# Performance work log

Hardware: AMD Instinct MI355X
Metric: run time of the kernel (lower is better)

Reference implementation:

```python
import jax, jax.numpy as jnp
import numpy as np

DT = 0.01
T, B, I, H, O = 512, 128, 256, 1024, 256


def setup_inputs() -> dict:
    key = jax.random.key(0)
    ks = jax.random.split(key, 9)
    def xavier(k, out_f, in_f):
        lim = np.sqrt(6.0 / (in_f + out_f)).astype(np.float32)
        return jax.random.uniform(k, (out_f, in_f), jnp.float32, -lim, lim)
    return {
        "x": jax.random.normal(ks[0], (T, B, I), jnp.float32),
        "W_h": xavier(ks[1], H, I + H),                      # HRCell linear, no bias
        "gain": jnp.ones((H,), jnp.float32),
        "omega": jax.random.uniform(ks[2], (H,), jnp.float32, 10.0, 50.0),
        "b_offset": jax.random.uniform(ks[3], (H,), jnp.float32, 1.0, 6.0),
        "W_o": xavier(ks[4], H, H),                          # LICell linear, no bias
        "tau_mem": 20.0 + 5.0 * jax.random.normal(ks[5], (H,), jnp.float32),
        "W_out": xavier(ks[6], O, H),                        # readout Linear
        "b_out": jnp.zeros((O,), jnp.float32),
    }


def reference(x, W_h, gain, omega, b_offset, W_o, tau_mem, W_out, b_out):
    om = jnp.abs(omega)
    om2 = om * om
    b = om2 * 0.005 + jnp.abs(b_offset)          # damping coefficient per unit
    alpha = jnp.exp(-1.0 / jnp.abs(tau_mem))     # leaky-integrator decay
    Bsz = x.shape[1]
    Hd = W_h.shape[0]
    Od = W_out.shape[0]

    def step(carry, x_t):
        hu, hv, ou, acc = carry
        # HRCell: linear on concat(input, hidden_u), then harmonic update
        in_sum = jnp.concatenate([x_t, hu], axis=1) @ W_h.T   # [B, H]
        hv = hv + hu * DT
        hu = hu + in_sum * DT - b * hu * (2.0 * DT) - om2 * hv * DT
        hu = hu * gain                                        # normalize=False path
        # LICell: leaky integrator on projected hidden
        ou = ou * alpha + (hu @ W_o.T) * (1.0 - alpha)
        # readout, summed over time
        acc = acc + ou @ W_out.T + b_out
        return (hu, hv, ou, acc), None

    z = jnp.zeros((Bsz, Hd), x.dtype)
    init = (z, z, z, jnp.zeros((Bsz, Od), x.dtype))
    (hu, hv, ou, acc), _ = jax.lax.scan(step, init, x)
    return acc
```

## Files before the change

kernel.cpp:

```cpp
#include <hip/hip_runtime.h>
#include <math.h>

#define DT 0.01f
constexpr int T = 512, B = 128, I = 256, H = 1024, O = 256;
constexpr int K = I + H;

constexpr size_t OFF_OSUM  = 0;
constexpr size_t OFF_HUH0  = OFF_OSUM + (size_t)B * H;
constexpr size_t OFF_HUL0  = OFF_HUH0 + (size_t)B * H / 2;
constexpr size_t OFF_HUH1  = OFF_HUL0 + (size_t)B * H / 2;
constexpr size_t OFF_HUL1  = OFF_HUH1 + (size_t)B * H / 2;
constexpr size_t OFF_COEF  = OFF_HUL1 + (size_t)B * H / 2;
constexpr size_t OFF_FLAGS = OFF_COEF + 5 * (size_t)H;
constexpr size_t OFF_WHH   = OFF_FLAGS + 8256;
constexpr size_t OFF_WHL   = OFF_WHH + 64 * 40 * 64 * 8 / 2;
constexpr size_t OFF_WOH   = OFF_WHL + 64 * 40 * 64 * 8 / 2;
constexpr size_t OFF_WOL   = OFF_WOH + 64 * 32 * 64 * 8 / 2;

constexpr int SM_WHH  = 0;
constexpr int SM_WHL  = 65536;
constexpr int SM_REDS = 131072;
constexpr int SM_REDP = 139520;
constexpr int SM_BYTES = 147968;

typedef __attribute__((ext_vector_type(8))) short short8v;
typedef __attribute__((ext_vector_type(4))) float f32x4;

static __device__ inline short f2bf(float f) {
    unsigned u = __builtin_bit_cast(unsigned, f);
    u += 0x7fffu + ((u >> 16) & 1u);
    return (short)(u >> 16);
}
static __device__ inline float bf2f(short s) {
    return __builtin_bit_cast(float, ((unsigned)(unsigned short)s) << 16);
}

__global__ __launch_bounds__(256)
void init_kernel(float* __restrict__ ws, const float* __restrict__ omega,
                 const float* __restrict__ b_offset, const float* __restrict__ tau_mem,
                 const float* __restrict__ gain) {
    size_t tid = (size_t)blockIdx.x * blockDim.x + threadIdx.x;
    size_t stride = (size_t)gridDim.x * blockDim.x;
    for (size_t i = tid; i < (size_t)B * H; i += stride) ws[OFF_HUH0 + i] = 0.0f;
    for (size_t i = tid; i < 8256; i += stride) ws[OFF_FLAGS + i] = 0.0f;
    if (tid < H) {
        float om  = fabsf(omega[tid]);
        float om2 = om * om;
        float bb  = om2 * 0.005f + fabsf(b_offset[tid]);
        float al  = expf(-1.0f / fabsf(tau_mem[tid]));
        float g   = gain[tid];
        ws[OFF_COEF + 0 * H + tid] = g * (1.0f - 2.0f * bb * DT);
        ws[OFF_COEF + 1 * H + tid] = g * DT;
        ws[OFF_COEF + 2 * H + tid] = g * om2 * DT;
        ws[OFF_COEF + 3 * H + tid] = al;
        ws[OFF_COEF + 4 * H + tid] = 1.0f - al;
    }
}

template <int NKS, int KD>
__global__ __launch_bounds__(256)
void convert_kernel(const float* __restrict__ W, short* __restrict__ WH,
                    short* __restrict__ WL) {
    int g = blockIdx.x * 256 + threadIdx.x;
    int lane = g & 63;
    int ks = (g >> 6) % NKS;
    int cg = g / (NKS * 64);
    int col = cg * 16 + (lane & 15);
    int k = ks * 32 + ((lane >> 4) << 3);
    const float* src = W + (size_t)col * KD + k;
    short8v hi, lo;
    #pragma unroll
    for (int j = 0; j < 8; ++j) {
        float v = src[j];
        short h = f2bf(v);
        hi[j] = h;
        lo[j] = f2bf(v - bf2f(h));
    }
    *(short8v*)(WH + (size_t)g * 8) = hi;
    *(short8v*)(WL + (size_t)g * 8) = lo;
}

__global__ __launch_bounds__(512)
void rnn_persist(const float* __restrict__ x, float* __restrict__ ws) {
    extern __shared__ char sm[];
    float* redS = (float*)(sm + SM_REDS);
    float* redP = (float*)(sm + SM_REDP);
    __shared__ int role_sm;

    const float* coef = ws + OFF_COEF;
    float* osum_g = ws + OFF_OSUM;
    const short* huhS[2] = {(const short*)(ws + OFF_HUH0), (const short*)(ws + OFF_HUH1)};
    const short* hulS[2] = {(const short*)(ws + OFF_HUL0), (const short*)(ws + OFF_HUL1)};
    unsigned int* huhW[2] = {(unsigned int*)(ws + OFF_HUH0), (unsigned int*)(ws + OFF_HUH1)};
    unsigned int* hulW[2] = {(unsigned int*)(ws + OFF_HUL0), (unsigned int*)(ws + OFF_HUL1)};
    int* flags = (int*)(ws + OFF_FLAGS);
    int* ctr   = flags + 8192;

    const int tid = threadIdx.x;

    if (tid == 0) {
        unsigned xcc_;
        asm volatile("s_getreg_b32 %0, hwreg(HW_REG_XCC_ID)" : "=s"(xcc_));
        int slot = atomicAdd(ctr + (xcc_ & 7), 1);
        role_sm = (int)((xcc_ & 7) * 32 + (slot & 31));
    }
    __syncthreads();
    const int role = role_sm;
    const int xcc = role >> 5;
    const int g   = role & 31;
    const int col0 = g * 32, row0 = xcc * 16;

    const int wid = tid >> 6, lane = tid & 63;
    const int ntile = wid & 1, ksl = wid >> 1;
    const int colgrp = 2 * g + ntile;
    const int rowg = row0 + (lane & 15);
    const int koff = (lane >> 4) << 3;

    {
        const float4* srcH = (const float4*)(ws + OFF_WHH);
        const float4* srcL = (const float4*)(ws + OFF_WHL);
        float4* dH = (float4*)(sm + SM_WHH);
        float4* dL = (float4*)(sm + SM_WHL);
        for (int i = tid; i < 2 * 2048; i += 512) {
            int n = i >> 11, rem = i & 2047;
            dH[i] = srcH[((size_t)(2 * g + n) * 40 + 8) * 64 + rem];
            dL[i] = srcL[((size_t)(2 * g + n) * 40 + 8) * 64 + rem];
        }
    }
    short8v woh[8], wxh[2], wxl[2];
    {
        const short8v* WOHg = (const short8v*)(ws + OFF_WOH) + (size_t)colgrp * 32 * 64 + lane;
        const short8v* WXH  = (const short8v*)(ws + OFF_WHH) + (size_t)colgrp * 40 * 64 + lane;
        const short8v* WXL  = (const short8v*)(ws + OFF_WHL) + (size_t)colgrp * 40 * 64 + lane;
        #pragma unroll
        for (int j = 0; j < 8; ++j) woh[j] = WOHg[(ksl * 8 + j) * 64];
        #pragma unroll
        for (int j = 0; j < 2; ++j) { wxh[j] = WXH[(ksl * 2 + j) * 64]; wxl[j] = WXL[(ksl * 2 + j) * 64]; }
    }
    __syncthreads();

    const short8v* lWHH = (const short8v*)(sm + SM_WHH) + (size_t)ntile * 2048 + lane;
    const short8v* lWHL = (const short8v*)(sm + SM_WHL) + (size_t)ntile * 2048 + lane;

    const int er = tid >> 4;
    const int ec0 = (tid & 15) * 2;
    const int gcol0 = col0 + ec0;
    const size_t erow = (size_t)(row0 + (er & 15));
    float k1a=0,k1b=0,k2a=0,k2b=0,k3a=0,k3b=0, ala=0,alb=0,alma=0,almb=0;
    if (tid < 256) {
        k1a = coef[gcol0];         k1b = coef[gcol0 + 1];
        k2a = coef[H + gcol0];     k2b = coef[H + gcol0 + 1];
        k3a = coef[2 * H + gcol0]; k3b = coef[2 * H + gcol0 + 1];
        ala = coef[3 * H + gcol0]; alb = coef[3 * H + gcol0 + 1];
        alma = coef[4 * H + gcol0]; almb = coef[4 * H + gcol0 + 1];
    }
    float hva=0,hvb=0,oua=0,oub=0,osa=0,osb=0,hua=0,hub=0;

    int* myfast = flags + ((xcc * 32 + g) << 4);
    int* mysafe = flags + 4096 + ((xcc * 32 + g) << 4);
    const int* fastp = flags + ((xcc * 32 + (tid & 31)) << 4);
    int* safep = flags + 4096 + ((xcc * 32 + (tid & 31)) << 4);
    const size_t rowOffH = (size_t)rowg * H + koff;

    for (int s = 0; s <= T; ++s) {
        const bool last = (s == T);
        f32x4 accS = {0,0,0,0}, accS2 = {0,0,0,0};
        f32x4 accP = {0,0,0,0}, accP2 = {0,0,0,0};

        if (!last) {
            const float* xrow = x + (size_t)s * B * I + (size_t)rowg * I + koff;
            #pragma unroll
            for (int j = 0; j < 2; ++j) {
                float4 a0 = *(const float4*)(xrow + (ksl * 2 + j) * 32);
                float4 a1 = *(const float4*)(xrow + (ksl * 2 + j) * 32 + 4);
                float av[8] = {a0.x,a0.y,a0.z,a0.w,a1.x,a1.y,a1.z,a1.w};
                short8v ah, alv;
                #pragma unroll
                for (int q = 0; q < 8; ++q) {
                    short h = f2bf(av[q]);
                    ah[q] = h;
                    alv[q] = f2bf(av[q] - bf2f(h));
                }
                f32x4* acc = j ? &accS2 : &accS;
                *acc = __builtin_amdgcn_mfma_f32_16x16x32_bf16(ah, wxh[j], *acc, 0,0,0);
                *acc = __builtin_amdgcn_mfma_f32_16x16x32_bf16(alv, wxh[j], *acc, 0,0,0);
                *acc = __builtin_amdgcn_mfma_f32_16x16x32_bf16(ah, wxl[j], *acc, 0,0,0);
            }
        }

        if (tid < 32) {
            int v, spins = 0;
            for (;;) {
                asm volatile("global_load_dword %0, %1, off sc0\n\ts_waitcnt vmcnt(0)"
                             : "=v"(v) : "v"(fastp) : "memory");
                if (v >= s) break;
                if ((++spins & 63) == 0) {
                    v = __hip_atomic_load(safep, __ATOMIC_RELAXED, __HIP_MEMORY_SCOPE_AGENT);
                    if (v >= s) break;
                }
                __builtin_amdgcn_s_sleep(1);
            }
        }
        __syncthreads();
        asm volatile("" ::: "memory");

        const short* hb_ = huhS[s & 1] + rowOffH;
        const short* lb_ = hulS[s & 1] + rowOffH;
        short8v hbuf[8], lbuf[8];
        #pragma unroll
        for (int j = 0; j < 8; ++j) {
            asm volatile("global_load_dwordx4 %0, %1, off sc0" : "=v"(hbuf[j]) : "v"(hb_ + (ksl * 8 + j) * 32));
            asm volatile("global_load_dwordx4 %0, %1, off sc0" : "=v"(lbuf[j]) : "v"(lb_ + (ksl * 8 + j) * 32));
        }
        if (s > 0 && tid < 256) {
            const float* rp = redP + er * 33 + ec0;
            float p0 = (rp[0] + rp[528]) + (rp[1056] + rp[1584]);
            float p1 = (rp[1] + rp[529]) + (rp[1057] + rp[1585]);
            oua = oua * ala + p0 * alma; osa += oua;
            oub = oub * alb + p1 * almb; osb += oub;
        }

        if (!last) {
            asm volatile("s_waitcnt vmcnt(8)");
            __builtin_amdgcn_sched_barrier(0);
            #pragma unroll
            for (int j = 0; j < 4; ++j) {
                short8v ch = lWHH[(ksl * 8 + j) * 64];
                short8v cl = lWHL[(ksl * 8 + j) * 64];
                f32x4* acc = (j & 1) ? &accS2 : &accS;
                *acc = __builtin_amdgcn_mfma_f32_16x16x32_bf16(hbuf[j], ch, *acc, 0,0,0);
                *acc = __builtin_amdgcn_mfma_f32_16x16x32_bf16(lbuf[j], ch, *acc, 0,0,0);
                *acc = __builtin_amdgcn_mfma_f32_16x16x32_bf16(hbuf[j], cl, *acc, 0,0,0);
            }
            asm volatile("s_waitcnt vmcnt(0)");
            __builtin_amdgcn_sched_barrier(0);
            #pragma unroll
            for (int j = 4; j < 8; ++j) {
                short8v ch = lWHH[(ksl * 8 + j) * 64];
                short8v cl = lWHL[(ksl * 8 + j) * 64];
                f32x4* acc = (j & 1) ? &accS2 : &accS;
                *acc = __builtin_amdgcn_mfma_f32_16x16x32_bf16(hbuf[j], ch, *acc, 0,0,0);
                *acc = __builtin_amdgcn_mfma_f32_16x16x32_bf16(lbuf[j], ch, *acc, 0,0,0);
                *acc = __builtin_amdgcn_mfma_f32_16x16x32_bf16(hbuf[j], cl, *acc, 0,0,0);
            }
            #pragma unroll
            for (int r = 0; r < 4; ++r) {
                int crow = ((lane >> 4) << 2) + r;
                redS[ksl * 528 + crow * 33 + ntile * 16 + (lane & 15)] = accS[r] + accS2[r];
            }
            __syncthreads();

            if (tid < 256) {
                const float* rs = redS + er * 33 + ec0;
                float s0 = (rs[0] + rs[528]) + (rs[1056] + rs[1584]);
                float s1 = (rs[1] + rs[529]) + (rs[1057] + rs[1585]);
                float hvn0 = hva + hua * DT;
                float hun0 = k1a * hua + k2a * s0 - k3a * hvn0;
                hva = hvn0; hua = hun0;
                float hvn1 = hvb + hub * DT;
                float hun1 = k1b * hub + k2b * s1 - k3b * hvn1;
                hvb = hvn1; hub = hun1;
                short h0 = f2bf(hun0), h1 = f2bf(hun1);
                short l0 = f2bf(hun0 - bf2f(h0)), l1 = f2bf(hun1 - bf2f(h1));
                unsigned hp = (unsigned)(unsigned short)h0 | ((unsigned)(unsigned short)h1 << 16);
                unsigned lp = (unsigned)(unsigned short)l0 | ((unsigned)(unsigned short)l1 << 16);
                size_t off32 = (erow * H + gcol0) >> 1;
                unsigned int* hp_ = huhW[(s + 1) & 1] + off32;
                unsigned int* lp_ = hulW[(s + 1) & 1] + off32;
                asm volatile("global_store_dword %0, %1, off sc0" :: "v"(hp_), "v"(hp) : "memory");
                asm volatile("global_store_dword %0, %1, off sc0" :: "v"(lp_), "v"(lp) : "memory");
            }
            asm volatile("s_waitcnt vmcnt(0)" ::: "memory");
            __syncthreads();
            if (tid == 0) {
                int fv = s + 1;
                asm volatile("global_store_dword %0, %1, off sc0" :: "v"(myfast), "v"(fv) : "memory");
                __hip_atomic_store(mysafe, fv, __ATOMIC_RELAXED, __HIP_MEMORY_SCOPE_AGENT);
            }
        } else {
            asm volatile("s_waitcnt vmcnt(0)");
            __builtin_amdgcn_sched_barrier(0);
            __syncthreads();
        }

        #pragma unroll
        for (int j = 0; j < 8; ++j) {
            f32x4* acc = (j & 1) ? &accP2 : &accP;
            *acc = __builtin_amdgcn_mfma_f32_16x16x32_bf16(hbuf[j], woh[j], *acc, 0,0,0);
            *acc = __builtin_amdgcn_mfma_f32_16x16x32_bf16(lbuf[j], woh[j], *acc, 0,0,0);
        }
        #pragma unroll
        for (int r = 0; r < 4; ++r) {
            int crow = ((lane >> 4) << 2) + r;
            redP[ksl * 528 + crow * 33 + ntile * 16 + (lane & 15)] = accP[r] + accP2[r];
        }
    }

    __syncthreads();
    if (tid < 256) {
        const float* rp = redP + er * 33 + ec0;
        float p0 = (rp[0] + rp[528]) + (rp[1056] + rp[1584]);
        float p1 = (rp[1] + rp[529]) + (rp[1057] + rp[1585]);
        float o0 = oua * ala + p0 * alma; osa += o0;
        float o1 = oub * alb + p1 * almb; osb += o1;
        osum_g[erow * H + gcol0] = osa;
        osum_g[erow * H + gcol0 + 1] = osb;
    }
}

__global__ __launch_bounds__(256)
void readout_kernel(const float* __restrict__ ou_sum, const float* __restrict__ W_out,
                    const float* __restrict__ b_out, float* __restrict__ out) {
    constexpr int KC = 128, BT = 32, CT = 16;
    __shared__ float act[BT][KC + 4];
    __shared__ float w[CT][KC + 4];
    int wg = blockIdx.x;
    int bt = wg & 3, cg = wg >> 2;
    int row0 = bt * BT, col0 = cg * CT;
    int tid = threadIdx.x;
    int c = tid & 15, rr = tid >> 4;

    float4 acc0 = {0, 0, 0, 0}, acc1 = {0, 0, 0, 0};
    for (int kc = 0; kc < H / KC; ++kc) {
        int k0 = kc * KC;
        for (int i = tid; i < BT * (KC / 4); i += 256) {
            int r = i >> 5, c4 = (i & 31) * 4;
            *(float4*)&act[r][c4] = *(const float4*)&ou_sum[(size_t)(row0 + r) * H + k0 + c4];
        }
        for (int i = tid; i < CT * (KC / 4); i += 256) {
            int r = i >> 5, c4 = (i & 31) * 4;
            *(float4*)&w[r][c4] = *(const float4*)&W_out[(size_t)(col0 + r) * H + k0 + c4];
        }
        __syncthreads();
        #pragma unroll
        for (int k4 = 0; k4 < KC / 4; ++k4) {
            float4 a0 = *(const float4*)&act[rr][k4 * 4];
            float4 a1 = *(const float4*)&act[rr + 16][k4 * 4];
            float4 w0 = *(const float4*)&w[c][k4 * 4];
            acc0.x = fmaf(a0.x, w0.x, acc0.x); acc0.y = fmaf(a0.y, w0.y, acc0.y);
            acc0.z = fmaf(a0.z, w0.z, acc0.z); acc0.w = fmaf(a0.w, w0.w, acc0.w);
            acc1.x = fmaf(a1.x, w0.x, acc1.x); acc1.y = fmaf(a1.y, w0.y, acc1.y);
            acc1.z = fmaf(a1.z, w0.z, acc1.z); acc1.w = fmaf(a1.w, w0.w, acc1.w);
        }
        __syncthreads();
    }
    float v0 = (acc0.x + acc0.y) + (acc0.z + acc0.w);
    float v1 = (acc1.x + acc1.y) + (acc1.z + acc1.w);
    int gcol = col0 + c;
    float bo = b_out[gcol] * (float)T;
    out[(size_t)(row0 + rr) * O + gcol] = v0 + bo;
    out[(size_t)(row0 + rr + 16) * O + gcol] = v1 + bo;
}

extern "C" void kernel_launch(void* const* d_in, const int* in_sizes, int n_in,
                              void* d_out, int out_size, void* d_ws, size_t ws_size,
                              hipStream_t stream) {
    const float* x        = (const float*)d_in[0];
    const float* W_h      = (const float*)d_in[1];
    const float* gain     = (const float*)d_in[2];
    const float* omega    = (const float*)d_in[3];
    const float* b_offset = (const float*)d_in[4];
    const float* W_o      = (const float*)d_in[5];
    const float* tau_mem  = (const float*)d_in[6];
    const float* W_out    = (const float*)d_in[7];
    const float* b_out    = (const float*)d_in[8];
    float* ws  = (float*)d_ws;
    float* out = (float*)d_out;

    init_kernel<<<512, 256, 0, stream>>>(ws, omega, b_offset, tau_mem, gain);
    convert_kernel<40, K><<<640, 256, 0, stream>>>(
        W_h, (short*)(ws + OFF_WHH), (short*)(ws + OFF_WHL));
    convert_kernel<32, H><<<512, 256, 0, stream>>>(
        W_o, (short*)(ws + OFF_WOH), (short*)(ws + OFF_WOL));

    rnn_persist<<<256, 512, SM_BYTES, stream>>>(x, ws);

    readout_kernel<<<64, 256, 0, stream>>>(ws + OFF_OSUM, W_out, b_out, out);
}
```

Before: 3.790 ms.

## Shrink persistent RNN blocks to two waves with full-K per wave and triple buffering

```diff
diff --git a/kernel.cpp b/kernel.cpp
--- a/kernel.cpp
+++ b/kernel.cpp
@@ -10,18 +10,16 @@
 constexpr size_t OFF_HUL0  = OFF_HUH0 + (size_t)B * H / 2;
 constexpr size_t OFF_HUH1  = OFF_HUL0 + (size_t)B * H / 2;
 constexpr size_t OFF_HUL1  = OFF_HUH1 + (size_t)B * H / 2;
-constexpr size_t OFF_COEF  = OFF_HUL1 + (size_t)B * H / 2;
+constexpr size_t OFF_HUH2  = OFF_HUL1 + (size_t)B * H / 2;
+constexpr size_t OFF_HUL2  = OFF_HUH2 + (size_t)B * H / 2;
+constexpr size_t OFF_COEF  = OFF_HUL2 + (size_t)B * H / 2;
 constexpr size_t OFF_FLAGS = OFF_COEF + 5 * (size_t)H;
-constexpr size_t OFF_WHH   = OFF_FLAGS + 8256;
+constexpr size_t OFF_WHH   = OFF_FLAGS + 9344;
 constexpr size_t OFF_WHL   = OFF_WHH + 64 * 40 * 64 * 8 / 2;
 constexpr size_t OFF_WOH   = OFF_WHL + 64 * 40 * 64 * 8 / 2;
 constexpr size_t OFF_WOL   = OFF_WOH + 64 * 32 * 64 * 8 / 2;
 
-constexpr int SM_WHH  = 0;
-constexpr int SM_WHL  = 65536;
-constexpr int SM_REDS = 131072;
-constexpr int SM_REDP = 139520;
-constexpr int SM_BYTES = 147968;
+constexpr int SM_BYTES = 131072;
 
 typedef __attribute__((ext_vector_type(8))) short short8v;
 typedef __attribute__((ext_vector_type(4))) float f32x4;
@@ -42,7 +40,7 @@
     size_t tid = (size_t)blockIdx.x * blockDim.x + threadIdx.x;
     size_t stride = (size_t)gridDim.x * blockDim.x;
     for (size_t i = tid; i < (size_t)B * H; i += stride) ws[OFF_HUH0 + i] = 0.0f;
-    for (size_t i = tid; i < 8256; i += stride) ws[OFF_FLAGS + i] = 0.0f;
+    for (size_t i = tid; i < 9344; i += stride) ws[OFF_FLAGS + i] = 0.0f;
     if (tid < H) {
         float om  = fabsf(omega[tid]);
         float om2 = om * om;
@@ -80,21 +78,21 @@
     *(short8v*)(WL + (size_t)g * 8) = lo;
 }
 
-__global__ __launch_bounds__(512)
+__global__ __launch_bounds__(128)
 void rnn_persist(const float* __restrict__ x, float* __restrict__ ws) {
     extern __shared__ char sm[];
-    float* redS = (float*)(sm + SM_REDS);
-    float* redP = (float*)(sm + SM_REDP);
     __shared__ int role_sm;
 
     const float* coef = ws + OFF_COEF;
     float* osum_g = ws + OFF_OSUM;
-    const short* huhS[2] = {(const short*)(ws + OFF_HUH0), (const short*)(ws + OFF_HUH1)};
-    const short* hulS[2] = {(const short*)(ws + OFF_HUL0), (const short*)(ws + OFF_HUL1)};
-    unsigned int* huhW[2] = {(unsigned int*)(ws + OFF_HUH0), (unsigned int*)(ws + OFF_HUH1)};
-    unsigned int* hulW[2] = {(unsigned int*)(ws + OFF_HUL0), (unsigned int*)(ws + OFF_HUL1)};
+    const short* huhS[3] = {(const short*)(ws + OFF_HUH0), (const short*)(ws + OFF_HUH1),
+                            (const short*)(ws + OFF_HUH2)};
+    const short* hulS[3] = {(const short*)(ws + OFF_HUL0), (const short*)(ws + OFF_HUL1),
+                            (const short*)(ws + OFF_HUL2)};
+    short* huhW[3] = {(short*)(ws + OFF_HUH0), (short*)(ws + OFF_HUH1), (short*)(ws + OFF_HUH2)};
+    short* hulW[3] = {(short*)(ws + OFF_HUL0), (short*)(ws + OFF_HUL1), (short*)(ws + OFF_HUL2)};
     int* flags = (int*)(ws + OFF_FLAGS);
-    int* ctr   = flags + 8192;
+    int* ctr   = flags + 9216;
 
     const int tid = threadIdx.x;
 
@@ -108,72 +106,60 @@
     const int role = role_sm;
     const int xcc = role >> 5;
     const int g   = role & 31;
-    const int col0 = g * 32, row0 = xcc * 16;
-
-    const int wid = tid >> 6, lane = tid & 63;
-    const int ntile = wid & 1, ksl = wid >> 1;
-    const int colgrp = 2 * g + ntile;
+    const int w   = tid >> 6, lane = tid & 63;
+    const int cg  = g * 2 + w;
+    const int col0 = cg * 16;
+    const int row0 = xcc * 16;
     const int rowg = row0 + (lane & 15);
     const int koff = (lane >> 4) << 3;
 
     {
         const float4* srcH = (const float4*)(ws + OFF_WHH);
         const float4* srcL = (const float4*)(ws + OFF_WHL);
-        float4* dH = (float4*)(sm + SM_WHH);
-        float4* dL = (float4*)(sm + SM_WHL);
-        for (int i = tid; i < 2 * 2048; i += 512) {
+        float4* dH = (float4*)sm;
+        float4* dL = (float4*)(sm + 65536);
+        for (int i = tid; i < 2 * 2048; i += 128) {
             int n = i >> 11, rem = i & 2047;
             dH[i] = srcH[((size_t)(2 * g + n) * 40 + 8) * 64 + rem];
             dL[i] = srcL[((size_t)(2 * g + n) * 40 + 8) * 64 + rem];
         }
     }
-    short8v woh[8], wxh[2], wxl[2];
+    short8v wxh[8], wxl[8];
     {
-        const short8v* WOHg = (const short8v*)(ws + OFF_WOH) + (size_t)colgrp * 32 * 64 + lane;
-        const short8v* WXH  = (const short8v*)(ws + OFF_WHH) + (size_t)colgrp * 40 * 64 + lane;
-        const short8v* WXL  = (const short8v*)(ws + OFF_WHL) + (size_t)colgrp * 40 * 64 + lane;
+        const short8v* WXH = (const short8v*)(ws + OFF_WHH) + (size_t)cg * 40 * 64 + lane;
+        const short8v* WXL = (const short8v*)(ws + OFF_WHL) + (size_t)cg * 40 * 64 + lane;
         #pragma unroll
-        for (int j = 0; j < 8; ++j) woh[j] = WOHg[(ksl * 8 + j) * 64];
-        #pragma unroll
-        for (int j = 0; j < 2; ++j) { wxh[j] = WXH[(ksl * 2 + j) * 64]; wxl[j] = WXL[(ksl * 2 + j) * 64]; }
+        for (int j = 0; j < 8; ++j) { wxh[j] = WXH[j * 64]; wxl[j] = WXL[j * 64]; }
     }
     __syncthreads();
 
-    const short8v* lWHH = (const short8v*)(sm + SM_WHH) + (size_t)ntile * 2048 + lane;
-    const short8v* lWHL = (const short8v*)(sm + SM_WHL) + (size_t)ntile * 2048 + lane;
-
-    const int er = tid >> 4;
-    const int ec0 = (tid & 15) * 2;
-    const int gcol0 = col0 + ec0;
-    const size_t erow = (size_t)(row0 + (er & 15));
-    float k1a=0,k1b=0,k2a=0,k2b=0,k3a=0,k3b=0, ala=0,alb=0,alma=0,almb=0;
-    if (tid < 256) {
-        k1a = coef[gcol0];         k1b = coef[gcol0 + 1];
-        k2a = coef[H + gcol0];     k2b = coef[H + gcol0 + 1];
-        k3a = coef[2 * H + gcol0]; k3b = coef[2 * H + gcol0 + 1];
-        ala = coef[3 * H + gcol0]; alb = coef[3 * H + gcol0 + 1];
-        alma = coef[4 * H + gcol0]; almb = coef[4 * H + gcol0 + 1];
-    }
-    float hva=0,hvb=0,oua=0,oub=0,osa=0,osb=0,hua=0,hub=0;
-
-    int* myfast = flags + ((xcc * 32 + g) << 4);
-    int* mysafe = flags + 4096 + ((xcc * 32 + g) << 4);
-    const int* fastp = flags + ((xcc * 32 + (tid & 31)) << 4);
-    int* safep = flags + 4096 + ((xcc * 32 + (tid & 31)) << 4);
-    const size_t rowOffH = (size_t)rowg * H + koff;
+    const short8v* lWHH = (const short8v*)sm + (size_t)w * 2048 + lane;
+    const short8v* lWHL = (const short8v*)(sm + 65536) + (size_t)w * 2048 + lane;
+    const short8v* WOH  = (const short8v*)(ws + OFF_WOH) + (size_t)cg * 32 * 64 + lane;
+
+    const int mycol = col0 + (lane & 15);
+    const int myrow0 = row0 + ((lane >> 4) << 2);
+    const float k1 = coef[mycol], k2 = coef[H + mycol], k3 = coef[2 * H + mycol];
+    const float al = coef[3 * H + mycol], alm = coef[4 * H + mycol];
+    float hu4[4] = {0,0,0,0}, hv4[4] = {0,0,0,0}, ou4[4] = {0,0,0,0}, os4[4] = {0,0,0,0};
+
+    int* myfast = flags + (xcc * 64 + cg);
+    int* mysafe = flags + 1024 + ((xcc * 64 + cg) << 4);
+    const int* pollfast = flags + (xcc * 64 + lane);
+    int* pollsafe = flags + 1024 + ((xcc * 64 + lane) << 4);
+    const size_t rowOff = (size_t)rowg * H + koff;
 
     for (int s = 0; s <= T; ++s) {
         const bool last = (s == T);
-        f32x4 accS = {0,0,0,0}, accS2 = {0,0,0,0};
-        f32x4 accP = {0,0,0,0}, accP2 = {0,0,0,0};
+        f32x4 a1 = {0,0,0,0}, a2 = {0,0,0,0}, a3 = {0,0,0,0};
 
         if (!last) {
             const float* xrow = x + (size_t)s * B * I + (size_t)rowg * I + koff;
             #pragma unroll
-            for (int j = 0; j < 2; ++j) {
-                float4 a0 = *(const float4*)(xrow + (ksl * 2 + j) * 32);
-                float4 a1 = *(const float4*)(xrow + (ksl * 2 + j) * 32 + 4);
-                float av[8] = {a0.x,a0.y,a0.z,a0.w,a1.x,a1.y,a1.z,a1.w};
+            for (int j = 0; j < 8; ++j) {
+                float4 q0 = *(const float4*)(xrow + j * 32);
+                float4 q1 = *(const float4*)(xrow + j * 32 + 4);
+                float av[8] = {q0.x,q0.y,q0.z,q0.w,q1.x,q1.y,q1.z,q1.w};
                 short8v ah, alv;
                 #pragma unroll
                 for (int q = 0; q < 8; ++q) {
@@ -181,131 +167,145 @@
                     ah[q] = h;
                     alv[q] = f2bf(av[q] - bf2f(h));
                 }
-                f32x4* acc = j ? &accS2 : &accS;
-                *acc = __builtin_amdgcn_mfma_f32_16x16x32_bf16(ah, wxh[j], *acc, 0,0,0);
-                *acc = __builtin_amdgcn_mfma_f32_16x16x32_bf16(alv, wxh[j], *acc, 0,0,0);
-                *acc = __builtin_amdgcn_mfma_f32_16x16x32_bf16(ah, wxl[j], *acc, 0,0,0);
-            }
-        }
-
-        if (tid < 32) {
+                a1 = __builtin_amdgcn_mfma_f32_16x16x32_bf16(ah,  wxh[j], a1, 0,0,0);
+                a2 = __builtin_amdgcn_mfma_f32_16x16x32_bf16(alv, wxh[j], a2, 0,0,0);
+                a3 = __builtin_amdgcn_mfma_f32_16x16x32_bf16(ah,  wxl[j], a3, 0,0,0);
+            }
+        }
+
+        {
             int v, spins = 0;
             for (;;) {
                 asm volatile("global_load_dword %0, %1, off sc0\n\ts_waitcnt vmcnt(0)"
-                             : "=v"(v) : "v"(fastp) : "memory");
-                if (v >= s) break;
+                             : "=v"(v) : "v"(pollfast) : "memory");
+                if (__all(v >= s)) break;
                 if ((++spins & 63) == 0) {
-                    v = __hip_atomic_load(safep, __ATOMIC_RELAXED, __HIP_MEMORY_SCOPE_AGENT);
-                    if (v >= s) break;
+                    int v2 = __hip_atomic_load(pollsafe, __ATOMIC_RELAXED, __HIP_MEMORY_SCOPE_AGENT);
+                    if (v2 > v) v = v2;
+                    if (__all(v >= s)) break;
                 }
                 __builtin_amdgcn_s_sleep(1);
             }
         }
-        __syncthreads();
         asm volatile("" ::: "memory");
 
-        const short* hb_ = huhS[s & 1] + rowOffH;
-        const short* lb_ = hulS[s & 1] + rowOffH;
-        short8v hbuf[8], lbuf[8];
-        #pragma unroll
-        for (int j = 0; j < 8; ++j) {
-            asm volatile("global_load_dwordx4 %0, %1, off sc0" : "=v"(hbuf[j]) : "v"(hb_ + (ksl * 8 + j) * 32));
-            asm volatile("global_load_dwordx4 %0, %1, off sc0" : "=v"(lbuf[j]) : "v"(lb_ + (ksl * 8 + j) * 32));
-        }
-        if (s > 0 && tid < 256) {
-            const float* rp = redP + er * 33 + ec0;
-            float p0 = (rp[0] + rp[528]) + (rp[1056] + rp[1584]);
-            float p1 = (rp[1] + rp[529]) + (rp[1057] + rp[1585]);
-            oua = oua * ala + p0 * alma; osa += oua;
-            oub = oub * alb + p1 * almb; osb += oub;
-        }
+        const short* hb = huhS[s % 3] + rowOff;
+        const short* lb = hulS[s % 3] + rowOff;
 
         if (!last) {
-            asm volatile("s_waitcnt vmcnt(8)");
+            short8v hA[8], lA[8], hB[8], lB[8];
+            #pragma unroll
+            for (int j = 0; j < 8; ++j) {
+                asm volatile("global_load_dwordx4 %0, %1, off sc0" : "=v"(hA[j]) : "v"(hb + j * 32));
+                asm volatile("global_load_dwordx4 %0, %1, off sc0" : "=v"(lA[j]) : "v"(lb + j * 32));
+            }
+            #pragma unroll
+            for (int j = 0; j < 8; ++j) {
+                asm volatile("global_load_dwordx4 %0, %1, off sc0" : "=v"(hB[j]) : "v"(hb + (8 + j) * 32));
+                asm volatile("global_load_dwordx4 %0, %1, off sc0" : "=v"(lB[j]) : "v"(lb + (8 + j) * 32));
+            }
+            asm volatile("s_waitcnt vmcnt(16)");
             __builtin_amdgcn_sched_barrier(0);
             #pragma unroll
-            for (int j = 0; j < 4; ++j) {
-                short8v ch = lWHH[(ksl * 8 + j) * 64];
-                short8v cl = lWHL[(ksl * 8 + j) * 64];
-                f32x4* acc = (j & 1) ? &accS2 : &accS;
-                *acc = __builtin_amdgcn_mfma_f32_16x16x32_bf16(hbuf[j], ch, *acc, 0,0,0);
-                *acc = __builtin_amdgcn_mfma_f32_16x16x32_bf16(lbuf[j], ch, *acc, 0,0,0);
-                *acc = __builtin_amdgcn_mfma_f32_16x16x32_bf16(hbuf[j], cl, *acc, 0,0,0);
+            for (int j = 0; j < 8; ++j) {
+                short8v ch = lWHH[j * 64], cl = lWHL[j * 64];
+                a1 = __builtin_amdgcn_mfma_f32_16x16x32_bf16(hA[j], ch, a1, 0,0,0);
+                a2 = __builtin_amdgcn_mfma_f32_16x16x32_bf16(lA[j], ch, a2, 0,0,0);
+                a3 = __builtin_amdgcn_mfma_f32_16x16x32_bf16(hA[j], cl, a3, 0,0,0);
+            }
+            #pragma unroll
+            for (int j = 0; j < 8; ++j) {
+                asm volatile("global_load_dwordx4 %0, %1, off sc0" : "=v"(hA[j]) : "v"(hb + (16 + j) * 32));
+                asm volatile("global_load_dwordx4 %0, %1, off sc0" : "=v"(lA[j]) : "v"(lb + (16 + j) * 32));
+            }
+            asm volatile("s_waitcnt vmcnt(16)");
+            __builtin_amdgcn_sched_barrier(0);
+            #pragma unroll
+            for (int j = 0; j < 8; ++j) {
+                short8v ch = lWHH[(8 + j) * 64], cl = lWHL[(8 + j) * 64];
+                a1 = __builtin_amdgcn_mfma_f32_16x16x32_bf16(hB[j], ch, a1, 0,0,0);
+                a2 = __builtin_amdgcn_mfma_f32_16x16x32_bf16(lB[j], ch, a2, 0,0,0);
+                a3 = __builtin_amdgcn_mfma_f32_16x16x32_bf16(hB[j], cl, a3, 0,0,0);
+            }
+            #pragma unroll
+            for (int j = 0; j < 8; ++j) {
+                asm volatile("global_load_dwordx4 %0, %1, off sc0" : "=v"(hB[j]) : "v"(hb + (24 + j) * 32));
+                asm volatile("global_load_dwordx4 %0, %1, off sc0" : "=v"(lB[j]) : "v"(lb + (24 + j) * 32));
+            }
+            asm volatile("s_waitcnt vmcnt(16)");
+            __builtin_amdgcn_sched_barrier(0);
+            #pragma unroll
+            for (int j = 0; j < 8; ++j) {
+                short8v ch = lWHH[(16 + j) * 64], cl = lWHL[(16 + j) * 64];
+                a1 = __builtin_amdgcn_mfma_f32_16x16x32_bf16(hA[j], ch, a1, 0,0,0);
+                a2 = __builtin_amdgcn_mfma_f32_16x16x32_bf16(lA[j], ch, a2, 0,0,0);
+                a3 = __builtin_amdgcn_mfma_f32_16x16x32_bf16(hA[j], cl, a3, 0,0,0);
             }
             asm volatile("s_waitcnt vmcnt(0)");
             __builtin_amdgcn_sched_barrier(0);
             #pragma unroll
-            for (int j = 4; j < 8; ++j) {
-                short8v ch = lWHH[(ksl * 8 + j) * 64];
-                short8v cl = lWHL[(ksl * 8 + j) * 64];
-                f32x4* acc = (j & 1) ? &accS2 : &accS;
-                *acc = __builtin_amdgcn_mfma_f32_16x16x32_bf16(hbuf[j], ch, *acc, 0,0,0);
-                *acc = __builtin_amdgcn_mfma_f32_16x16x32_bf16(lbuf[j], ch, *acc, 0,0,0);
-                *acc = __builtin_amdgcn_mfma_f32_16x16x32_bf16(hbuf[j], cl, *acc, 0,0,0);
-            }
+            for (int j = 0; j < 8; ++j) {
+                short8v ch = lWHH[(24 + j) * 64], cl = lWHL[(24 + j) * 64];
+                a1 = __builtin_amdgcn_mfma_f32_16x16x32_bf16(hB[j], ch, a1, 0,0,0);
+                a2 = __builtin_amdgcn_mfma_f32_16x16x32_bf16(lB[j], ch, a2, 0,0,0);
+                a3 = __builtin_amdgcn_mfma_f32_16x16x32_bf16(hB[j], cl, a3, 0,0,0);
+            }
+
+            short* hp = huhW[(s + 1) % 3];
+            short* lp = hulW[(s + 1) % 3];
             #pragma unroll
             for (int r = 0; r < 4; ++r) {
-                int crow = ((lane >> 4) << 2) + r;
-                redS[ksl * 528 + crow * 33 + ntile * 16 + (lane & 15)] = accS[r] + accS2[r];
-            }
-            __syncthreads();
-
-            if (tid < 256) {
-                const float* rs = redS + er * 33 + ec0;
-                float s0 = (rs[0] + rs[528]) + (rs[1056] + rs[1584]);
-                float s1 = (rs[1] + rs[529]) + (rs[1057] + rs[1585]);
-                float hvn0 = hva + hua * DT;
-                float hun0 = k1a * hua + k2a * s0 - k3a * hvn0;
-                hva = hvn0; hua = hun0;
-                float hvn1 = hvb + hub * DT;
-                float hun1 = k1b * hub + k2b * s1 - k3b * hvn1;
-                hvb = hvn1; hub = hun1;
-                short h0 = f2bf(hun0), h1 = f2bf(hun1);
-                short l0 = f2bf(hun0 - bf2f(h0)), l1 = f2bf(hun1 - bf2f(h1));
-                unsigned hp = (unsigned)(unsigned short)h0 | ((unsigned)(unsigned short)h1 << 16);
-                unsigned lp = (unsigned)(unsigned short)l0 | ((unsigned)(unsigned short)l1 << 16);
-                size_t off32 = (erow * H + gcol0) >> 1;
-                unsigned int* hp_ = huhW[(s + 1) & 1] + off32;
-                unsigned int* lp_ = hulW[(s + 1) & 1] + off32;
-                asm volatile("global_store_dword %0, %1, off sc0" :: "v"(hp_), "v"(hp) : "memory");
-                asm volatile("global_store_dword %0, %1, off sc0" :: "v"(lp_), "v"(lp) : "memory");
+                float si = (a1[r] + a2[r]) + a3[r];
+                float hvn = hv4[r] + hu4[r] * DT;
+                float hun = k1 * hu4[r] + k2 * si - k3 * hvn;
+                hv4[r] = hvn;
+                hu4[r] = hun;
+                short hh = f2bf(hun);
+                short ll = f2bf(hun - bf2f(hh));
+                size_t ix = (size_t)(myrow0 + r) * H + mycol;
+                unsigned hv_ = (unsigned short)hh, lv_ = (unsigned short)ll;
+                asm volatile("global_store_short %0, %1, off sc0" :: "v"(hp + ix), "v"(hv_) : "memory");
+                asm volatile("global_store_short %0, %1, off sc0" :: "v"(lp + ix), "v"(lv_) : "memory");
             }
             asm volatile("s_waitcnt vmcnt(0)" ::: "memory");
-            __syncthreads();
-            if (tid == 0) {
+            if (lane == 0) {
                 int fv = s + 1;
                 asm volatile("global_store_dword %0, %1, off sc0" :: "v"(myfast), "v"(fv) : "memory");
                 __hip_atomic_store(mysafe, fv, __ATOMIC_RELAXED, __HIP_MEMORY_SCOPE_AGENT);
             }
-        } else {
-            asm volatile("s_waitcnt vmcnt(0)");
-            __builtin_amdgcn_sched_barrier(0);
-            __syncthreads();
-        }
-
-        #pragma unroll
-        for (int j = 0; j < 8; ++j) {
-            f32x4* acc = (j & 1) ? &accP2 : &accP;
-            *acc = __builtin_amdgcn_mfma_f32_16x16x32_bf16(hbuf[j], woh[j], *acc, 0,0,0);
-            *acc = __builtin_amdgcn_mfma_f32_16x16x32_bf16(lbuf[j], woh[j], *acc, 0,0,0);
-        }
-        #pragma unroll
-        for (int r = 0; r < 4; ++r) {
-            int crow = ((lane >> 4) << 2) + r;
-            redP[ksl * 528 + crow * 33 + ntile * 16 + (lane & 15)] = accP[r] + accP2[r];
-        }
-    }
-
-    __syncthreads();
-    if (tid < 256) {
-        const float* rp = redP + er * 33 + ec0;
-        float p0 = (rp[0] + rp[528]) + (rp[1056] + rp[1584]);
-        float p1 = (rp[1] + rp[529]) + (rp[1057] + rp[1585]);
-        float o0 = oua * ala + p0 * alma; osa += o0;
-        float o1 = oub * alb + p1 * almb; osb += o1;
-        osum_g[erow * H + gcol0] = osa;
-        osum_g[erow * H + gcol0 + 1] = osb;
-    }
+        }
+
+        {
+            f32x4 p1 = {0,0,0,0}, p2 = {0,0,0,0};
+            for (int b = 0; b < 4; ++b) {
+                short8v hh8[8], ll8[8];
+                #pragma unroll
+                for (int j = 0; j < 8; ++j) {
+                    int ks = b * 8 + j;
+                    asm volatile("global_load_dwordx4 %0, %1, off sc0" : "=v"(hh8[j]) : "v"(hb + ks * 32));
+                    asm volatile("global_load_dwordx4 %0, %1, off sc0" : "=v"(ll8[j]) : "v"(lb + ks * 32));
+                }
+                asm volatile("s_waitcnt vmcnt(0)");
+                __builtin_amdgcn_sched_barrier(0);
+                #pragma unroll
+                for (int j = 0; j < 8; ++j) {
+                    short8v wo = WOH[(b * 8 + j) * 64];
+                    p1 = __builtin_amdgcn_mfma_f32_16x16x32_bf16(hh8[j], wo, p1, 0,0,0);
+                    p2 = __builtin_amdgcn_mfma_f32_16x16x32_bf16(ll8[j], wo, p2, 0,0,0);
+                }
+            }
+            #pragma unroll
+            for (int r = 0; r < 4; ++r) {
+                float q = p1[r] + p2[r];
+                ou4[r] = al * ou4[r] + alm * q;
+                os4[r] += ou4[r];
+            }
+        }
+    }
+
+    #pragma unroll
+    for (int r = 0; r < 4; ++r)
+        osum_g[(size_t)(myrow0 + r) * H + mycol] = os4[r];
 }
 
 __global__ __launch_bounds__(256)
@@ -373,7 +373,7 @@
     convert_kernel<32, H><<<512, 256, 0, stream>>>(
         W_o, (short*)(ws + OFF_WOH), (short*)(ws + OFF_WOL));
 
-    rnn_persist<<<256, 512, SM_BYTES, stream>>>(x, ws);
+    rnn_persist<<<256, 128, SM_BYTES, stream>>>(x, ws);
 
     readout_kernel<<<64, 256, 0, stream>>>(ws + OFF_OSUM, W_out, b_out, out);
 }
```

Result: slower. 6.708 ms (+77.0%).
